# Kernel tuning notes

Measured on AMD Instinct MI355X. Metric: run time of the kernel, lower is better.

## Reference

```python
import jax, jax.numpy as jnp
import numpy as np

SIZE = (96, 128, 160)  # (D, H, W)


def _make_grid():
    # Matches NSETransformer.__init__: normalized, aspect-preserving grid in [-1,1]
    vs = [np.arange(s, dtype=np.float32) for s in SIZE]
    g = np.stack(np.meshgrid(*vs, indexing='ij')).astype(np.float32)  # (3,D,H,W)
    mx = max(SIZE) - 1
    for i, s in enumerate(SIZE):
        g[i] = 2.0 * (g[i] / (s - 1) - 0.5) * (s - 1) / mx
    return jnp.asarray(g)


def _grid_sample_3d_border(src, coords):
    # src: (1,C,D,H,W); coords: (1,D,H,W,3) with last dim (x,y,z) indexing (W,H,D)
    # align_corners=True, padding_mode='border', trilinear
    C = src.shape[1]
    D, H, W = src.shape[2], src.shape[3], src.shape[4]
    v = src[0]  # (C,D,H,W)
    x, y, z = coords[0, ..., 0], coords[0, ..., 1], coords[0, ..., 2]
    ix = jnp.clip((x + 1.0) * 0.5 * (W - 1), 0.0, W - 1)
    iy = jnp.clip((y + 1.0) * 0.5 * (H - 1), 0.0, H - 1)
    iz = jnp.clip((z + 1.0) * 0.5 * (D - 1), 0.0, D - 1)
    x0 = jnp.floor(ix).astype(jnp.int32); x1 = jnp.minimum(x0 + 1, W - 1)
    y0 = jnp.floor(iy).astype(jnp.int32); y1 = jnp.minimum(y0 + 1, H - 1)
    z0 = jnp.floor(iz).astype(jnp.int32); z1 = jnp.minimum(z0 + 1, D - 1)
    wx = ix - x0.astype(ix.dtype)
    wy = iy - y0.astype(iy.dtype)
    wz = iz - z0.astype(iz.dtype)
    out = jnp.zeros((C,) + x.shape, src.dtype)
    for zi, wz_ in ((z0, 1.0 - wz), (z1, wz)):
        for yi, wy_ in ((y0, 1.0 - wy), (y1, wy)):
            for xi, wx_ in ((x0, 1.0 - wx), (x1, wx)):
                out = out + v[:, zi, yi, xi] * (wz_ * wy_ * wx_)
    return out[None]  # (1,C,D,H,W)


def reference(src, flow):
    # src: (1,D,H,W,C); flow: (D*H*W, 7) = [tx,ty,tz,qx,qy,qz,qw] per voxel (lietorch SE3)
    D, H, W = SIZE
    grid = _make_grid()  # (3,D,H,W)
    pts = grid.transpose(1, 2, 3, 0).reshape(-1, 3)  # (N,3)
    t, qv, qw = flow[:, :3], flow[:, 3:6], flow[:, 6:7]
    # SE3 act with unit quaternion: p' = p + 2*qv x (qv x p + qw*p) + t
    uv = jnp.cross(qv, pts) + qw * pts
    new_loc = (pts + 2.0 * jnp.cross(qv, uv) + t).reshape(1, D, H, W, 3)
    mx = max(SIZE) - 1
    scale = jnp.array([(s - 1) / mx for s in SIZE], dtype=new_loc.dtype)
    new_locs = (new_loc / scale)[..., ::-1]  # axis flip [2,1,0] -> (x,y,z) order
    vol = src.reshape(1, D, H, W, -1).transpose(0, 4, 1, 2, 3)  # (1,C,D,H,W)
    warped = _grid_sample_3d_border(vol, new_locs)
    return warped, new_loc.transpose(0, 4, 1, 2, 3), grid[None]


def setup_inputs() -> dict:
    key = jax.random.key(0)
    k1, k2, k3 = jax.random.split(key, 3)
    D, H, W = SIZE
    N = D * H * W
    src = jax.random.normal(k1, (1, D, H, W, 2), dtype=jnp.float32)
    t = jax.random.normal(k2, (N, 3), dtype=jnp.float32) * 0.05
    q = jax.random.normal(k3, (N, 4), dtype=jnp.float32)
    q = q / jnp.linalg.norm(q, axis=-1, keepdims=True)  # unit quaternions
    flow = jnp.concatenate([t, q], axis=-1)  # (N,7)
    return {"src": src, "flow": flow}
```

## Files before the change

### kernel.cpp

```cpp
#include <hip/hip_runtime.h>
#include <hip/hip_fp16.h>

#define DD 96
#define HH 128
#define WW 160
#define HW (HH * WW)
#define NN (DD * HH * WW)
#define BLK 256
#define PTS 2

__global__ __launch_bounds__(256) void pack4_kernel(
    const float2* __restrict__ src, uint4* __restrict__ vol)
{
    int n = blockIdx.x * blockDim.x + threadIdx.x;
    if (n >= NN) return;
    int rem = n % HW;
    int y = rem / WW;
    int x = rem % WW;
    int dy = (y < HH - 1) ? WW : 0;
    int dx = (x < WW - 1) ? 1 : 0;
    float2 a = src[n];
    float2 b = src[n + dy];
    float2 c = src[n + dx];
    float2 d = src[n + dy + dx];
    uint4 e;
    e.x = __builtin_bit_cast(unsigned int, __floats2half2_rn(a.x, a.y));
    e.y = __builtin_bit_cast(unsigned int, __floats2half2_rn(b.x, b.y));
    e.z = __builtin_bit_cast(unsigned int, __floats2half2_rn(c.x, c.y));
    e.w = __builtin_bit_cast(unsigned int, __floats2half2_rn(d.x, d.y));
    vol[n] = e;
}

__global__ __launch_bounds__(256) void warp3d_quad2_kernel(
    const uint4* __restrict__ vol,
    const float* __restrict__ flow,
    float* __restrict__ out)
{
    __shared__ float fsh[BLK * PTS * 7];
    int t = threadIdx.x;
    int base = blockIdx.x * (BLK * PTS);
    const float* fb = flow + (size_t)base * 7;
    #pragma unroll
    for (int k = 0; k < 7 * PTS; ++k)
        fsh[k * BLK + t] = __builtin_nontemporal_load(fb + k * BLK + t);
    __syncthreads();

    float ixs[PTS], iys[PTS], izs[PTS];
    uint4 g0[PTS], g1[PTS];

    const float inv_mx = 1.0f / 159.0f;

    #pragma unroll
    for (int j = 0; j < PTS; ++j) {
        int n = base + j * BLK + t;
        int w  = n % WW;
        int hd = n / WW;
        int h  = hd % HH;
        int d  = hd / HH;

        float p0 = (float)(2 * d - (DD - 1)) * inv_mx;
        float p1 = (float)(2 * h - (HH - 1)) * inv_mx;
        float p2 = (float)(2 * w - (WW - 1)) * inv_mx;

        const float* fl = &fsh[(t + j * BLK) * 7];
        float t0 = fl[0], t1 = fl[1], t2 = fl[2];
        float q0 = fl[3], q1 = fl[4], q2 = fl[5], qw = fl[6];

        float u0 = q1 * p2 - q2 * p1 + qw * p0;
        float u1 = q2 * p0 - q0 * p2 + qw * p1;
        float u2 = q0 * p1 - q1 * p0 + qw * p2;
        float nl0 = p0 + 2.0f * (q1 * u2 - q2 * u1) + t0;
        float nl1 = p1 + 2.0f * (q2 * u0 - q0 * u2) + t1;
        float nl2 = p2 + 2.0f * (q0 * u1 - q1 * u0) + t2;

        __builtin_nontemporal_store(nl0, out + 2 * NN + n);
        __builtin_nontemporal_store(nl1, out + 3 * NN + n);
        __builtin_nontemporal_store(nl2, out + 4 * NN + n);
        __builtin_nontemporal_store(p0,  out + 5 * NN + n);
        __builtin_nontemporal_store(p1,  out + 6 * NN + n);
        __builtin_nontemporal_store(p2,  out + 7 * NN + n);

        float ix = fminf(fmaxf(nl2 * 79.5f + 79.5f, 0.0f), (float)(WW - 1));
        float iy = fminf(fmaxf(nl1 * 79.5f + 63.5f, 0.0f), (float)(HH - 1));
        float iz = fminf(fmaxf(nl0 * 79.5f + 47.5f, 0.0f), (float)(DD - 1));
        ixs[j] = ix; iys[j] = iy; izs[j] = iz;

        int x0 = min((int)ix, WW - 2);
        int y0 = min((int)iy, HH - 2);
        int z0 = min((int)iz, DD - 2);
        size_t e0 = (size_t)(z0 * HH + y0) * WW + x0;
        g0[j] = vol[e0];
        g1[j] = vol[e0 + HW];
    }

    #pragma unroll
    for (int j = 0; j < PTS; ++j) {
        int n = base + j * BLK + t;
        float ix = ixs[j], iy = iys[j], iz = izs[j];
        int x0 = min((int)ix, WW - 2);
        int y0 = min((int)iy, HH - 2);
        int z0 = min((int)iz, DD - 2);
        float wx = ix - (float)x0;
        float wy = iy - (float)y0;
        float wz = iz - (float)z0;

        float wx1 = 1.0f - wx, wy1 = 1.0f - wy, wz1 = 1.0f - wz;
        float w00 = wy1 * wx1;
        float w10 = wy  * wx1;
        float w01 = wy1 * wx;
        float w11 = wy  * wx;

        float2 a00 = __half22float2(__builtin_bit_cast(__half2, g0[j].x));
        float2 a10 = __half22float2(__builtin_bit_cast(__half2, g0[j].y));
        float2 a01 = __half22float2(__builtin_bit_cast(__half2, g0[j].z));
        float2 a11 = __half22float2(__builtin_bit_cast(__half2, g0[j].w));
        float2 b00 = __half22float2(__builtin_bit_cast(__half2, g1[j].x));
        float2 b10 = __half22float2(__builtin_bit_cast(__half2, g1[j].y));
        float2 b01 = __half22float2(__builtin_bit_cast(__half2, g1[j].z));
        float2 b11 = __half22float2(__builtin_bit_cast(__half2, g1[j].w));

        float s0 = a00.x * w00 + a10.x * w10 + a01.x * w01 + a11.x * w11;
        float s1 = a00.y * w00 + a10.y * w10 + a01.y * w01 + a11.y * w11;
        float r0 = b00.x * w00 + b10.x * w10 + b01.x * w01 + b11.x * w11;
        float r1 = b00.y * w00 + b10.y * w10 + b01.y * w01 + b11.y * w11;

        float o0 = wz1 * s0 + wz * r0;
        float o1 = wz1 * s1 + wz * r1;

        __builtin_nontemporal_store(o0, out + n);
        __builtin_nontemporal_store(o1, out + NN + n);
    }
}

__global__ __launch_bounds__(256) void compress_kernel(
    const float2* __restrict__ src, __half2* __restrict__ vol)
{
    int n = blockIdx.x * blockDim.x + threadIdx.x;
    if (n >= NN) return;
    float2 v = src[n];
    vol[n] = __floats2half2_rn(v.x, v.y);
}

__global__ __launch_bounds__(256) void warp3d_fp16_kernel(
    const __half2* __restrict__ vol, const float* __restrict__ flow,
    float* __restrict__ out)
{
    int n = blockIdx.x * blockDim.x + threadIdx.x;
    if (n >= NN) return;
    int w  = n % WW;
    int hd = n / WW;
    int h  = hd % HH;
    int d  = hd / HH;
    const float inv_mx = 1.0f / 159.0f;
    float p0 = (float)(2 * d - (DD - 1)) * inv_mx;
    float p1 = (float)(2 * h - (HH - 1)) * inv_mx;
    float p2 = (float)(2 * w - (WW - 1)) * inv_mx;
    const float* f = flow + (size_t)n * 7;
    float t0 = f[0], t1 = f[1], t2 = f[2];
    float q0 = f[3], q1 = f[4], q2 = f[5], qw = f[6];
    float u0 = q1 * p2 - q2 * p1 + qw * p0;
    float u1 = q2 * p0 - q0 * p2 + qw * p1;
    float u2 = q0 * p1 - q1 * p0 + qw * p2;
    float nl0 = p0 + 2.0f * (q1 * u2 - q2 * u1) + t0;
    float nl1 = p1 + 2.0f * (q2 * u0 - q0 * u2) + t1;
    float nl2 = p2 + 2.0f * (q0 * u1 - q1 * u0) + t2;
    float ix = fminf(fmaxf(nl2 * 79.5f + 79.5f, 0.0f), (float)(WW - 1));
    float iy = fminf(fmaxf(nl1 * 79.5f + 63.5f, 0.0f), (float)(HH - 1));
    float iz = fminf(fmaxf(nl0 * 79.5f + 47.5f, 0.0f), (float)(DD - 1));
    int x0 = (int)floorf(ix); int x1 = min(x0 + 1, WW - 1);
    int y0 = (int)floorf(iy); int y1 = min(y0 + 1, HH - 1);
    int z0 = (int)floorf(iz); int z1 = min(z0 + 1, DD - 1);
    float wx = ix - (float)x0, wy = iy - (float)y0, wz = iz - (float)z0;
    int b00 = (z0 * HH + y0) * WW;
    int b01 = (z0 * HH + y1) * WW;
    int b10 = (z1 * HH + y0) * WW;
    int b11 = (z1 * HH + y1) * WW;
    float2 c000 = __half22float2(vol[b00 + x0]);
    float2 c001 = __half22float2(vol[b00 + x1]);
    float2 c010 = __half22float2(vol[b01 + x0]);
    float2 c011 = __half22float2(vol[b01 + x1]);
    float2 c100 = __half22float2(vol[b10 + x0]);
    float2 c101 = __half22float2(vol[b10 + x1]);
    float2 c110 = __half22float2(vol[b11 + x0]);
    float2 c111 = __half22float2(vol[b11 + x1]);
    float wx1 = 1.0f - wx, wy1 = 1.0f - wy, wz1 = 1.0f - wz;
    float w000 = wz1*wy1*wx1, w001 = wz1*wy1*wx, w010 = wz1*wy*wx1, w011 = wz1*wy*wx;
    float w100 = wz*wy1*wx1,  w101 = wz*wy1*wx,  w110 = wz*wy*wx1,  w111 = wz*wy*wx;
    float o0 = c000.x*w000 + c001.x*w001 + c010.x*w010 + c011.x*w011
             + c100.x*w100 + c101.x*w101 + c110.x*w110 + c111.x*w111;
    float o1 = c000.y*w000 + c001.y*w001 + c010.y*w010 + c011.y*w011
             + c100.y*w100 + c101.y*w101 + c110.y*w110 + c111.y*w111;
    out[n] = o0;
    out[NN + n] = o1;
    out[2*NN + n] = nl0; out[3*NN + n] = nl1; out[4*NN + n] = nl2;
    out[5*NN + n] = p0;  out[6*NN + n] = p1;  out[7*NN + n] = p2;
}

__global__ __launch_bounds__(256) void warp3d_fp32_kernel(
    const float* __restrict__ src, const float* __restrict__ flow,
    float* __restrict__ out)
{
    int n = blockIdx.x * blockDim.x + threadIdx.x;
    if (n >= NN) return;
    int w  = n % WW;
    int hd = n / WW;
    int h  = hd % HH;
    int d  = hd / HH;
    const float inv_mx = 1.0f / 159.0f;
    float p0 = (float)(2 * d - (DD - 1)) * inv_mx;
    float p1 = (float)(2 * h - (HH - 1)) * inv_mx;
    float p2 = (float)(2 * w - (WW - 1)) * inv_mx;
    const float* f = flow + (size_t)n * 7;
    float t0 = f[0], t1 = f[1], t2 = f[2];
    float q0 = f[3], q1 = f[4], q2 = f[5], qw = f[6];
    float u0 = q1 * p2 - q2 * p1 + qw * p0;
    float u1 = q2 * p0 - q0 * p2 + qw * p1;
    float u2 = q0 * p1 - q1 * p0 + qw * p2;
    float nl0 = p0 + 2.0f * (q1 * u2 - q2 * u1) + t0;
    float nl1 = p1 + 2.0f * (q2 * u0 - q0 * u2) + t1;
    float nl2 = p2 + 2.0f * (q0 * u1 - q1 * u0) + t2;
    float ix = fminf(fmaxf(nl2 * 79.5f + 79.5f, 0.0f), (float)(WW - 1));
    float iy = fminf(fmaxf(nl1 * 79.5f + 63.5f, 0.0f), (float)(HH - 1));
    float iz = fminf(fmaxf(nl0 * 79.5f + 47.5f, 0.0f), (float)(DD - 1));
    int x0 = (int)floorf(ix); int x1 = min(x0 + 1, WW - 1);
    int y0 = (int)floorf(iy); int y1 = min(y0 + 1, HH - 1);
    int z0 = (int)floorf(iz); int z1 = min(z0 + 1, DD - 1);
    float wx = ix - (float)x0, wy = iy - (float)y0, wz = iz - (float)z0;
    const float2* v = (const float2*)src;
    int b00 = (z0 * HH + y0) * WW;
    int b01 = (z0 * HH + y1) * WW;
    int b10 = (z1 * HH + y0) * WW;
    int b11 = (z1 * HH + y1) * WW;
    float2 c000 = v[b00 + x0], c001 = v[b00 + x1];
    float2 c010 = v[b01 + x0], c011 = v[b01 + x1];
    float2 c100 = v[b10 + x0], c101 = v[b10 + x1];
    float2 c110 = v[b11 + x0], c111 = v[b11 + x1];
    float wx1 = 1.0f - wx, wy1 = 1.0f - wy, wz1 = 1.0f - wz;
    float w000 = wz1*wy1*wx1, w001 = wz1*wy1*wx, w010 = wz1*wy*wx1, w011 = wz1*wy*wx;
    float w100 = wz*wy1*wx1,  w101 = wz*wy1*wx,  w110 = wz*wy*wx1,  w111 = wz*wy*wx;
    float o0 = c000.x*w000 + c001.x*w001 + c010.x*w010 + c011.x*w011
             + c100.x*w100 + c101.x*w101 + c110.x*w110 + c111.x*w111;
    float o1 = c000.y*w000 + c001.y*w001 + c010.y*w010 + c011.y*w011
             + c100.y*w100 + c101.y*w101 + c110.y*w110 + c111.y*w111;
    out[n] = o0;
    out[NN + n] = o1;
    out[2*NN + n] = nl0; out[3*NN + n] = nl1; out[4*NN + n] = nl2;
    out[5*NN + n] = p0;  out[6*NN + n] = p1;  out[7*NN + n] = p2;
}

extern "C" void kernel_launch(void* const* d_in, const int* in_sizes, int n_in,
                              void* d_out, int out_size, void* d_ws, size_t ws_size,
                              hipStream_t stream) {
    const float* src  = (const float*)d_in[0];
    const float* flow = (const float*)d_in[1];
    float* out = (float*)d_out;
    dim3 block(BLK);
    if (ws_size >= (size_t)NN * sizeof(uint4)) {
        uint4* vol = (uint4*)d_ws;
        pack4_kernel<<<dim3(NN / BLK), block, 0, stream>>>((const float2*)src, vol);
        warp3d_quad2_kernel<<<dim3(NN / (BLK * PTS)), block, 0, stream>>>(vol, flow, out);
    } else if (ws_size >= (size_t)NN * sizeof(__half2)) {
        __half2* vol = (__half2*)d_ws;
        compress_kernel<<<dim3(NN / BLK), block, 0, stream>>>((const float2*)src, vol);
        warp3d_fp16_kernel<<<dim3(NN / BLK), block, 0, stream>>>(vol, flow, out);
    } else {
        warp3d_fp32_kernel<<<dim3(NN / BLK), block, 0, stream>>>(src, flow, out);
    }
}
```

Before: 172.4 us.

## Pack full 2x2x2 corner cube per voxel into contiguous 32-byte entries

The pack kernel now stores all eight fp16 trilinear corners of each voxel as two adjacent uint4 values, where it used to store four corners. The gather then reads one contiguous 32-byte span per sample instead of two loads a plane apart, which should improve cache-line locality for the random gathers. The cost is doubling the packed volume size and the pack kernel's write traffic, plus a workspace requirement of 32 bytes per voxel. Points per thread also rise from 2 to 4, which adds memory-level parallelism but raises register pressure.

```diff
diff --git a/kernel.cpp b/kernel.cpp
--- a/kernel.cpp
+++ b/kernel.cpp
@@ -7,31 +7,44 @@
 #define HW (HH * WW)
 #define NN (DD * HH * WW)
 #define BLK 256
-#define PTS 2
-
-__global__ __launch_bounds__(256) void pack4_kernel(
+#define PTS 4
+
+__global__ __launch_bounds__(256) void pack8_kernel(
     const float2* __restrict__ src, uint4* __restrict__ vol)
 {
     int n = blockIdx.x * blockDim.x + threadIdx.x;
     if (n >= NN) return;
+    int z   = n / HW;
     int rem = n % HW;
     int y = rem / WW;
     int x = rem % WW;
     int dy = (y < HH - 1) ? WW : 0;
     int dx = (x < WW - 1) ? 1 : 0;
-    float2 a = src[n];
-    float2 b = src[n + dy];
-    float2 c = src[n + dx];
-    float2 d = src[n + dy + dx];
-    uint4 e;
-    e.x = __builtin_bit_cast(unsigned int, __floats2half2_rn(a.x, a.y));
-    e.y = __builtin_bit_cast(unsigned int, __floats2half2_rn(b.x, b.y));
-    e.z = __builtin_bit_cast(unsigned int, __floats2half2_rn(c.x, c.y));
-    e.w = __builtin_bit_cast(unsigned int, __floats2half2_rn(d.x, d.y));
-    vol[n] = e;
-}
-
-__global__ __launch_bounds__(256) void warp3d_quad2_kernel(
+    int dz = (z < DD - 1) ? HW : 0;
+
+    float2 a00 = src[n];
+    float2 a10 = src[n + dy];
+    float2 a01 = src[n + dx];
+    float2 a11 = src[n + dy + dx];
+    float2 b00 = src[n + dz];
+    float2 b10 = src[n + dz + dy];
+    float2 b01 = src[n + dz + dx];
+    float2 b11 = src[n + dz + dy + dx];
+
+    uint4 e0, e1;
+    e0.x = __builtin_bit_cast(unsigned int, __floats2half2_rn(a00.x, a00.y));
+    e0.y = __builtin_bit_cast(unsigned int, __floats2half2_rn(a10.x, a10.y));
+    e0.z = __builtin_bit_cast(unsigned int, __floats2half2_rn(a01.x, a01.y));
+    e0.w = __builtin_bit_cast(unsigned int, __floats2half2_rn(a11.x, a11.y));
+    e1.x = __builtin_bit_cast(unsigned int, __floats2half2_rn(b00.x, b00.y));
+    e1.y = __builtin_bit_cast(unsigned int, __floats2half2_rn(b10.x, b10.y));
+    e1.z = __builtin_bit_cast(unsigned int, __floats2half2_rn(b01.x, b01.y));
+    e1.w = __builtin_bit_cast(unsigned int, __floats2half2_rn(b11.x, b11.y));
+    vol[2 * (size_t)n]     = e0;
+    vol[2 * (size_t)n + 1] = e1;
+}
+
+__global__ __launch_bounds__(256) void warp3d_cube_kernel(
     const uint4* __restrict__ vol,
     const float* __restrict__ flow,
     float* __restrict__ out)
@@ -88,9 +101,9 @@
         int x0 = min((int)ix, WW - 2);
         int y0 = min((int)iy, HH - 2);
         int z0 = min((int)iz, DD - 2);
-        size_t e0 = (size_t)(z0 * HH + y0) * WW + x0;
-        g0[j] = vol[e0];
-        g1[j] = vol[e0 + HW];
+        size_t e = ((size_t)(z0 * HH + y0) * WW + x0) * 2;
+        g0[j] = vol[e];
+        g1[j] = vol[e + 1];
     }
 
     #pragma unroll
@@ -255,10 +268,10 @@
     const float* flow = (const float*)d_in[1];
     float* out = (float*)d_out;
     dim3 block(BLK);
-    if (ws_size >= (size_t)NN * sizeof(uint4)) {
+    if (ws_size >= (size_t)NN * 32) {
         uint4* vol = (uint4*)d_ws;
-        pack4_kernel<<<dim3(NN / BLK), block, 0, stream>>>((const float2*)src, vol);
-        warp3d_quad2_kernel<<<dim3(NN / (BLK * PTS)), block, 0, stream>>>(vol, flow, out);
+        pack8_kernel<<<dim3(NN / BLK), block, 0, stream>>>((const float2*)src, vol);
+        warp3d_cube_kernel<<<dim3(NN / (BLK * PTS)), block, 0, stream>>>(vol, flow, out);
     } else if (ws_size >= (size_t)NN * sizeof(__half2)) {
         __half2* vol = (__half2*)d_ws;
         compress_kernel<<<dim3(NN / BLK), block, 0, stream>>>((const float2*)src, vol);
```

New measurement: 163.0 us. 5.4% less time.
